# Kernel optimization log

Measured on AMD Instinct MI355X. Metric: run time of the kernel, lower is better.

Reference implementation:

```python
import jax, jax.numpy as jnp
import numpy as np

DIM = 1024
HEADS = 16
HEAD_DIM = DIM // HEADS
THETA = 10000.0


def _freqs_cis(d, n, theta=THETA):
    # complex rotary frequencies, shape (n, d//2)
    pos = jnp.arange(n, dtype=jnp.float32)
    inv = 1.0 / theta ** (jnp.arange(0, d, 2, dtype=jnp.float32) / d)
    ang = jnp.outer(pos, inv)
    return jax.lax.complex(jnp.cos(ang), jnp.sin(ang))


def _to_complex(x):
    # (..., d) -> (..., d//2) complex via adjacent pairs
    xr = x.astype(jnp.float32).reshape(*x.shape[:-1], -1, 2)
    return jax.lax.complex(xr[..., 0], xr[..., 1])


def _to_real(xc):
    # (..., d//2) complex -> (..., d) interleaved real/imag
    return jnp.stack([jnp.real(xc), jnp.imag(xc)], axis=-1).reshape(*xc.shape[:-1], -1)


def setup_inputs() -> dict:
    key = jax.random.key(0)
    k1, k2, k3 = jax.random.split(key, 3)
    b, seq = 2, 2048
    x = jax.random.normal(k1, (b, DIM, seq), dtype=jnp.float32)
    w_qkv = jax.random.normal(k2, (3 * DIM, DIM), dtype=jnp.float32) * (DIM ** -0.5)
    w_out = jax.random.normal(k3, (DIM, DIM), dtype=jnp.float32) * (DIM ** -0.5)
    return {"x": x, "w_qkv": w_qkv, "w_out": w_out}


def reference(x, w_qkv, w_out):
    b, dim, n = x.shape
    h, hd = HEADS, HEAD_DIM
    scale = hd ** -0.5
    xt = jnp.swapaxes(x, -1, -2)                      # (b, t, dim)
    qkv = jnp.einsum('btd,ed->bte', xt, w_qkv)        # (b, t, 3*dim)
    q, k, v = jnp.split(qkv, 3, axis=-1)
    q = q.reshape(b, n, h, hd)
    k = k.reshape(b, n, h, hd)
    v = v.reshape(b, n, h, hd)
    # rotary embedding on q, k
    fc = _freqs_cis(hd, n)[None, :, None, :]          # (1, t, 1, hd//2)
    q = _to_real(_to_complex(q) * fc).astype(x.dtype)
    k = _to_real(_to_complex(k) * fc).astype(x.dtype)
    # naive full attention
    logits = jnp.einsum('bqhd,bkhd->bhqk', q, k) * scale
    probs = jax.nn.softmax(logits, axis=-1)
    out = jnp.einsum('bhqk,bkhd->bqhd', probs, v)     # (b, t, h, hd)
    out = out.reshape(b, n, dim)
    out = jnp.einsum('btd,ed->bte', out, w_out)       # (b, t, dim)
    return jnp.swapaxes(out, -1, -2)                  # (b, dim, t)
```

## Files before the change

kernel.cpp:

```cpp
#include <hip/hip_runtime.h>
#include <hip/hip_bf16.h>
#include <math.h>

#define B 2
#define N 2048
#define D 1024
#define H 16
#define HD 64

typedef __attribute__((ext_vector_type(8))) short short8;
typedef __attribute__((ext_vector_type(4))) float f32x4;
typedef __attribute__((ext_vector_type(16))) float f32x16;
typedef __attribute__((ext_vector_type(4))) unsigned short ush4;
typedef __attribute__((ext_vector_type(4))) unsigned int uint4v;

__device__ __forceinline__ float bf2f(unsigned short u) {
  unsigned int x = ((unsigned int)u) << 16;
  float f;
  __builtin_memcpy(&f, &x, 4);
  return f;
}
__device__ __forceinline__ unsigned short f2bf(float f) {
  unsigned int x;
  __builtin_memcpy(&x, &f, 4);
  x = x + 0x7fffu + ((x >> 16) & 1u);
  return (unsigned short)(x >> 16);
}
__device__ __forceinline__ unsigned int pk2(float lo, float hi) {
  union { __hip_bfloat162 h; unsigned int u; } cv;
  cv.h = __float22bfloat162_rn(make_float2(lo, hi));
  return cv.u;
}
__device__ __forceinline__ short8 mk_frag(unsigned int w0, unsigned int w1,
                                          unsigned int w2, unsigned int w3) {
  union { uint4v u; short8 s; } cv;
  cv.u = (uint4v){w0, w1, w2, w3};
  return cv.s;
}

__device__ __forceinline__ void gload16(const unsigned short* g, unsigned short* l) {
  __builtin_amdgcn_global_load_lds(
      (const __attribute__((address_space(1))) unsigned int*)(const void*)g,
      (__attribute__((address_space(3))) unsigned int*)(void*)l, 16, 0, 0);
}

__global__ void conv_bf16(const float* __restrict__ src, unsigned short* __restrict__ dst, int n4) {
  int i = blockIdx.x * 256 + threadIdx.x;
  if (i >= n4) return;
  float4 v = ((const float4*)src)[i];
  ush4 o;
  o[0] = f2bf(v.x); o[1] = f2bf(v.y); o[2] = f2bf(v.z); o[3] = f2bf(v.w);
  *(ush4*)&dst[i * 4] = o;
}

__global__ __launch_bounds__(256) void transpose_x(const float* __restrict__ x,
                                                   unsigned short* __restrict__ xt) {
  __shared__ float tile[32][33];
  const int tx = threadIdx.x, ty = threadIdx.y;
  const int t0 = blockIdx.x * 32, d0 = blockIdx.y * 32, bb = blockIdx.z;
#pragma unroll
  for (int i = 0; i < 4; ++i) {
    int r = ty * 4 + i;
    tile[r][tx] = x[(size_t)bb * D * N + (size_t)(d0 + r) * N + t0 + tx];
  }
  __syncthreads();
#pragma unroll
  for (int i = 0; i < 4; ++i) {
    int r = ty * 4 + i;
    xt[((size_t)(bb * N) + t0 + r) * D + d0 + tx] = f2bf(tile[tx][r]);
  }
}

__global__ void rope_table(float2* __restrict__ tab) {
  int idx = blockIdx.x * 256 + threadIdx.x;
  int t = idx >> 5, p = idx & 31;
  float inv = powf(10000.f, -(float)p / 32.f);
  float ang = (float)t * inv;
  float s, c;
  sincosf(ang, &s, &c);
  tab[idx] = make_float2(c, s);
}

template <int MODE>
__global__ __launch_bounds__(256) void gemm_bt(const unsigned short* __restrict__ A,
                                               const unsigned short* __restrict__ Bt,
                                               float* __restrict__ outf,
                                               unsigned short* __restrict__ qkbuf,
                                               unsigned short* __restrict__ vtbuf) {
  __shared__ unsigned short Asm[128 * 64];
  __shared__ unsigned short Bsm[128 * 64];
  const int tid = threadIdx.x;
  const int lane = tid & 63, wid = tid >> 6;
  const int ln = lane & 15, lh = lane >> 4;
  const int wr = wid >> 1, wc = wid & 1;
  const int m0 = blockIdx.x * 128, n0 = blockIdx.y * 128;

  f32x4 acc[4][4];
#pragma unroll
  for (int i = 0; i < 4; ++i)
#pragma unroll
    for (int j = 0; j < 4; ++j) acc[i][j] = (f32x4){0.f, 0.f, 0.f, 0.f};

  for (int k0 = 0; k0 < 1024; k0 += 64) {
#pragma unroll
    for (int jj = 0; jj < 4; ++jj) {
      int slot = tid + jj * 256;
      int row = slot >> 3, u = slot & 7;
      int usw = (u ^ (row & 7)) * 8;
      gload16(&A[(size_t)(m0 + row) * 1024 + k0 + usw], &Asm[slot * 8]);
    }
#pragma unroll
    for (int jj = 0; jj < 4; ++jj) {
      int slot = tid + jj * 256;
      int row = slot >> 3, u = slot & 7;
      int usw = (u ^ (row & 7)) * 8;
      gload16(&Bt[(size_t)(n0 + row) * 1024 + k0 + usw], &Bsm[slot * 8]);
    }
    __syncthreads();
#pragma unroll
    for (int s = 0; s < 2; ++s) {
      short8 af[4], bfr[4];
#pragma unroll
      for (int i = 0; i < 4; ++i) {
        int row = wr * 64 + i * 16 + ln;
        int u = ((s * 4 + lh) ^ (row & 7)) * 8;
        af[i] = *(const short8*)&Asm[row * 64 + u];
      }
#pragma unroll
      for (int j = 0; j < 4; ++j) {
        int row = wc * 64 + j * 16 + ln;
        int u = ((s * 4 + lh) ^ (row & 7)) * 8;
        bfr[j] = *(const short8*)&Bsm[row * 64 + u];
      }
#pragma unroll
      for (int i = 0; i < 4; ++i)
#pragma unroll
        for (int j = 0; j < 4; ++j)
          acc[i][j] = __builtin_amdgcn_mfma_f32_16x16x32_bf16(af[i], bfr[j], acc[i][j], 0, 0, 0);
    }
    __syncthreads();
  }

#pragma unroll
  for (int i = 0; i < 4; ++i) {
    int mrow = m0 + wr * 64 + i * 16 + lh * 4;
    int bb = mrow >> 11, t = mrow & 2047;
#pragma unroll
    for (int j = 0; j < 4; ++j) {
      int e = n0 + wc * 64 + j * 16 + ln;
      if (MODE == 1) {
        float* op = outf + (size_t)bb * D * N + (size_t)e * N + t;
        *(f32x4*)op = acc[i][j];
      } else {
        if (e < 2048) {
#pragma unroll
          for (int jj = 0; jj < 4; ++jj)
            qkbuf[((size_t)(bb * N + t + jj)) * 2048 + e] = f2bf(acc[i][j][jj]);
        } else {
          ush4 v;
#pragma unroll
          for (int jj = 0; jj < 4; ++jj) v[jj] = f2bf(acc[i][j][jj]);
          *(ush4*)&vtbuf[((size_t)bb * 1024 + (e - 2048)) * N + t] = v;
        }
      }
    }
  }
}

__global__ void rope_kernel(unsigned short* __restrict__ qk, const float2* __restrict__ tab) {
  int idx = blockIdx.x * 256 + threadIdx.x;
  int e = (idx & 255) * 8;
  int t = (idx >> 8) & 2047;
  int bb = idx >> 19;
  int p0 = (e & 63) >> 1;
  const float qscl = 0.125f * 1.4426950408889634f;
  float sc = (e < 1024) ? qscl : 1.0f;
  unsigned short* p = qk + ((size_t)(bb * N + t)) * 2048 + e;
  short8 v = *(short8*)p;
#pragma unroll
  for (int q = 0; q < 4; ++q) {
    float2 cs = tab[t * 32 + p0 + q];
    float xe = bf2f((unsigned short)v[2 * q]);
    float xo = bf2f((unsigned short)v[2 * q + 1]);
    v[2 * q] = (short)f2bf((xe * cs.x - xo * cs.y) * sc);
    v[2 * q + 1] = (short)f2bf((xe * cs.y + xo * cs.x) * sc);
  }
  *(short8*)p = v;
}

__global__ __launch_bounds__(256, 2) void attn_kernel(const unsigned short* __restrict__ qk,
                                                      const unsigned short* __restrict__ vt,
                                                      unsigned short* __restrict__ ob) {
  __shared__ unsigned short Ksm[2][64 * 64];
  __shared__ unsigned short Vsm[2][64 * 64];
  const int tid = threadIdx.x;
  const int lane = tid & 63, wid = tid >> 6;
  const int l31 = lane & 31, hi = lane >> 5;
  const int L = blockIdx.x;
  const int hh = L & 31, qb = L >> 5;
  const int bb = hh >> 4, h = hh & 15;
  const unsigned short* Qg = qk + (size_t)bb * N * 2048 + h * 64;
  const unsigned short* Kg = Qg + 1024;
  const unsigned short* Vg = vt + ((size_t)bb * 1024 + h * 64) * N;

  const int q = qb * 128 + wid * 32 + l31;
  short8 qf[4];
#pragma unroll
  for (int c = 0; c < 4; ++c)
    qf[c] = *(const short8*)&Qg[(size_t)q * 2048 + c * 16 + hi * 8];

  f32x16 oL, oH;
#pragma unroll
  for (int r = 0; r < 16; ++r) { oL[r] = 0.f; oH[r] = 0.f; }
  float lrun = 0.f;

  auto STAGE = [&](int buf, int kb) {
#pragma unroll
    for (int jj = 0; jj < 2; ++jj) {
      int slot = tid + jj * 256;
      int row = slot >> 3, u = slot & 7;
      int usw = (u ^ (row & 7)) * 8;
      gload16(&Kg[(size_t)(kb + row) * 2048 + usw], &Ksm[buf][slot * 8]);
    }
#pragma unroll
    for (int jj = 0; jj < 2; ++jj) {
      int slot = tid + jj * 256;
      int row = slot >> 3, u = slot & 7;
      int usw = (u ^ (row & 7)) * 8;
      gload16(&Vg[(size_t)row * N + kb + usw], &Vsm[buf][slot * 8]);
    }
  };

  STAGE(0, 0);
  __syncthreads();
  int cur = 0;
  for (int t = 0; t < N / 64; ++t) {
    if (t < N / 64 - 1) STAGE(cur ^ 1, (t + 1) * 64);
    f32x16 s0, s1;
#pragma unroll
    for (int r = 0; r < 16; ++r) { s0[r] = 0.f; s1[r] = 0.f; }
#pragma unroll
    for (int c = 0; c < 4; ++c) {
      short8 ka = *(const short8*)&Ksm[cur][l31 * 64 + (((c * 2 + hi) ^ (l31 & 7)) * 8)];
      s0 = __builtin_amdgcn_mfma_f32_32x32x16_bf16(ka, qf[c], s0, 0, 0, 0);
      int r1 = 32 + l31;
      short8 kb2 = *(const short8*)&Ksm[cur][r1 * 64 + (((c * 2 + hi) ^ (r1 & 7)) * 8)];
      s1 = __builtin_amdgcn_mfma_f32_32x32x16_bf16(kb2, qf[c], s1, 0, 0, 0);
    }
    float lsum = 0.f;
#pragma unroll
    for (int r = 0; r < 16; ++r) {
      s0[r] = __builtin_amdgcn_exp2f(s0[r]);
      s1[r] = __builtin_amdgcn_exp2f(s1[r]);
      lsum += s0[r] + s1[r];
    }
    lrun += lsum;
    unsigned int W[16];
#pragma unroll
    for (int i = 0; i < 8; ++i) {
      W[i] = pk2(s0[2 * i], s0[2 * i + 1]);
      W[8 + i] = pk2(s1[2 * i], s1[2 * i + 1]);
    }
    short8 pf[4];
#pragma unroll
    for (int c = 0; c < 4; ++c) {
      unsigned int a0 = W[4 * c + 0], b0 = W[4 * c + 2];
      unsigned int a1 = W[4 * c + 1], b1 = W[4 * c + 3];
      asm volatile("v_permlane32_swap_b32 %0, %1" : "+v"(a0), "+v"(b0));
      asm volatile("v_permlane32_swap_b32 %0, %1" : "+v"(a1), "+v"(b1));
      pf[c] = mk_frag(a0, a1, b0, b1);
    }
#pragma unroll
    for (int c = 0; c < 4; ++c) {
      short8 va = *(const short8*)&Vsm[cur][l31 * 64 + (((c * 2 + hi) ^ (l31 & 7)) * 8)];
      oL = __builtin_amdgcn_mfma_f32_32x32x16_bf16(va, pf[c], oL, 0, 0, 0);
      int rH = 32 + l31;
      short8 vb = *(const short8*)&Vsm[cur][rH * 64 + (((c * 2 + hi) ^ (rH & 7)) * 8)];
      oH = __builtin_amdgcn_mfma_f32_32x32x16_bf16(vb, pf[c], oH, 0, 0, 0);
    }
    __syncthreads();
    cur ^= 1;
  }
  lrun += __shfl_xor(lrun, 32, 64);
  float inv = 1.f / lrun;
  unsigned short* obp = ob + ((size_t)(bb * N + q)) * 1024 + h * 64;
#pragma unroll
  for (int r4 = 0; r4 < 4; ++r4) {
    ush4 vL, vH;
#pragma unroll
    for (int i = 0; i < 4; ++i) {
      vL[i] = f2bf(oL[r4 * 4 + i] * inv);
      vH[i] = f2bf(oH[r4 * 4 + i] * inv);
    }
    *(ush4*)&obp[r4 * 8 + hi * 4] = vL;
    *(ush4*)&obp[32 + r4 * 8 + hi * 4] = vH;
  }
}

extern "C" void kernel_launch(void* const* d_in, const int* in_sizes, int n_in,
                              void* d_out, int out_size, void* d_ws, size_t ws_size,
                              hipStream_t stream) {
  const float* x = (const float*)d_in[0];
  const float* w_qkv = (const float*)d_in[1];
  const float* w_out = (const float*)d_in[2];
  float* out = (float*)d_out;
  char* ws = (char*)d_ws;

  unsigned short* wqkv_bf = (unsigned short*)ws;
  unsigned short* wout_bf = (unsigned short*)(ws + 6291456);
  unsigned short* xt      = (unsigned short*)(ws + 8388608);
  unsigned short* qkbuf   = (unsigned short*)(ws + 16777216);
  unsigned short* vtbuf   = (unsigned short*)(ws + 33554432);
  float2* tab             = (float2*)(ws + 41943040);

  conv_bf16<<<3072, 256, 0, stream>>>(w_qkv, wqkv_bf, 3072 * 1024 / 4);
  conv_bf16<<<1024, 256, 0, stream>>>(w_out, wout_bf, 1024 * 1024 / 4);
  transpose_x<<<dim3(N / 32, D / 32, B), dim3(32, 8), 0, stream>>>(x, xt);
  rope_table<<<256, 256, 0, stream>>>(tab);

  gemm_bt<0><<<dim3(32, 24), 256, 0, stream>>>(xt, wqkv_bf, nullptr, qkbuf, vtbuf);
  rope_kernel<<<4096, 256, 0, stream>>>(qkbuf, tab);
  attn_kernel<<<512, 256, 0, stream>>>(qkbuf, vtbuf, xt );
  gemm_bt<1><<<dim3(32, 8), 256, 0, stream>>>(xt, wout_bf, out, nullptr, nullptr);
}
```

Measured before the change: 132.8 us.

## Triple-buffer attention K/V loads with explicit waitcnt and fuse prep kernels

The attention loop moves from double to triple-buffered K/V staging. Each tile is prefetched two iterations ahead, using s_waitcnt vmcnt plus raw s_barrier instead of __syncthreads, and setprio raises priority around the MFMA blocks. The weight conversion and rope table kernels are merged into one launch. This is meant to hide global load latency and cut launch overhead, at the cost of 50% more LDS per block and fragile hand-counted wait counts.

```diff
diff --git a/kernel.cpp b/kernel.cpp
--- a/kernel.cpp
+++ b/kernel.cpp
@@ -44,13 +44,27 @@
       (__attribute__((address_space(3))) unsigned int*)(void*)l, 16, 0, 0);
 }
 
-__global__ void conv_bf16(const float* __restrict__ src, unsigned short* __restrict__ dst, int n4) {
-  int i = blockIdx.x * 256 + threadIdx.x;
-  if (i >= n4) return;
-  float4 v = ((const float4*)src)[i];
-  ush4 o;
-  o[0] = f2bf(v.x); o[1] = f2bf(v.y); o[2] = f2bf(v.z); o[3] = f2bf(v.w);
-  *(ush4*)&dst[i * 4] = o;
+__global__ void prep_k(const float* __restrict__ wqkv, unsigned short* __restrict__ wqkv_bf,
+                       const float* __restrict__ wout, unsigned short* __restrict__ wout_bf,
+                       float2* __restrict__ tab) {
+  int blk = blockIdx.x;
+  if (blk < 4096) {
+    const float* src = (blk < 3072) ? wqkv : wout;
+    unsigned short* dst = (blk < 3072) ? wqkv_bf : wout_bf;
+    int i = (blk < 3072 ? blk : blk - 3072) * 256 + threadIdx.x;
+    float4 v = ((const float4*)src)[i];
+    ush4 o;
+    o[0] = f2bf(v.x); o[1] = f2bf(v.y); o[2] = f2bf(v.z); o[3] = f2bf(v.w);
+    *(ush4*)&dst[i * 4] = o;
+  } else {
+    int idx = (blk - 4096) * 256 + threadIdx.x;
+    int t = idx >> 5, p = idx & 31;
+    float inv = powf(10000.f, -(float)p / 32.f);
+    float ang = (float)t * inv;
+    float s, c;
+    sincosf(ang, &s, &c);
+    tab[idx] = make_float2(c, s);
+  }
 }
 
 __global__ __launch_bounds__(256) void transpose_x(const float* __restrict__ x,
@@ -69,16 +83,6 @@
     int r = ty * 4 + i;
     xt[((size_t)(bb * N) + t0 + r) * D + d0 + tx] = f2bf(tile[tx][r]);
   }
-}
-
-__global__ void rope_table(float2* __restrict__ tab) {
-  int idx = blockIdx.x * 256 + threadIdx.x;
-  int t = idx >> 5, p = idx & 31;
-  float inv = powf(10000.f, -(float)p / 32.f);
-  float ang = (float)t * inv;
-  float s, c;
-  sincosf(ang, &s, &c);
-  tab[idx] = make_float2(c, s);
 }
 
 template <int MODE>
@@ -191,8 +195,8 @@
 __global__ __launch_bounds__(256, 2) void attn_kernel(const unsigned short* __restrict__ qk,
                                                       const unsigned short* __restrict__ vt,
                                                       unsigned short* __restrict__ ob) {
-  __shared__ unsigned short Ksm[2][64 * 64];
-  __shared__ unsigned short Vsm[2][64 * 64];
+  __shared__ unsigned short Ksm[3][64 * 64];
+  __shared__ unsigned short Vsm[3][64 * 64];
   const int tid = threadIdx.x;
   const int lane = tid & 63, wid = tid >> 6;
   const int l31 = lane & 31, hi = lane >> 5;
@@ -214,39 +218,37 @@
   for (int r = 0; r < 16; ++r) { oL[r] = 0.f; oH[r] = 0.f; }
   float lrun = 0.f;
 
-  auto STAGE = [&](int buf, int kb) {
+  auto STAGE = [&](unsigned short* Kb, unsigned short* Vb, int kb) {
 #pragma unroll
     for (int jj = 0; jj < 2; ++jj) {
       int slot = tid + jj * 256;
       int row = slot >> 3, u = slot & 7;
       int usw = (u ^ (row & 7)) * 8;
-      gload16(&Kg[(size_t)(kb + row) * 2048 + usw], &Ksm[buf][slot * 8]);
+      gload16(&Kg[(size_t)(kb + row) * 2048 + usw], &Kb[slot * 8]);
     }
 #pragma unroll
     for (int jj = 0; jj < 2; ++jj) {
       int slot = tid + jj * 256;
       int row = slot >> 3, u = slot & 7;
       int usw = (u ^ (row & 7)) * 8;
-      gload16(&Vg[(size_t)row * N + kb + usw], &Vsm[buf][slot * 8]);
+      gload16(&Vg[(size_t)row * N + kb + usw], &Vb[slot * 8]);
     }
   };
 
-  STAGE(0, 0);
-  __syncthreads();
-  int cur = 0;
-  for (int t = 0; t < N / 64; ++t) {
-    if (t < N / 64 - 1) STAGE(cur ^ 1, (t + 1) * 64);
+  auto COMPUTE = [&](const unsigned short* Kb, const unsigned short* Vb) {
     f32x16 s0, s1;
 #pragma unroll
     for (int r = 0; r < 16; ++r) { s0[r] = 0.f; s1[r] = 0.f; }
+    __builtin_amdgcn_s_setprio(1);
 #pragma unroll
     for (int c = 0; c < 4; ++c) {
-      short8 ka = *(const short8*)&Ksm[cur][l31 * 64 + (((c * 2 + hi) ^ (l31 & 7)) * 8)];
+      short8 ka = *(const short8*)&Kb[l31 * 64 + (((c * 2 + hi) ^ (l31 & 7)) * 8)];
       s0 = __builtin_amdgcn_mfma_f32_32x32x16_bf16(ka, qf[c], s0, 0, 0, 0);
       int r1 = 32 + l31;
-      short8 kb2 = *(const short8*)&Ksm[cur][r1 * 64 + (((c * 2 + hi) ^ (r1 & 7)) * 8)];
+      short8 kb2 = *(const short8*)&Kb[r1 * 64 + (((c * 2 + hi) ^ (r1 & 7)) * 8)];
       s1 = __builtin_amdgcn_mfma_f32_32x32x16_bf16(kb2, qf[c], s1, 0, 0, 0);
     }
+    __builtin_amdgcn_s_setprio(0);
     float lsum = 0.f;
 #pragma unroll
     for (int r = 0; r < 16; ++r) {
@@ -270,17 +272,44 @@
       asm volatile("v_permlane32_swap_b32 %0, %1" : "+v"(a1), "+v"(b1));
       pf[c] = mk_frag(a0, a1, b0, b1);
     }
+    __builtin_amdgcn_s_setprio(1);
 #pragma unroll
     for (int c = 0; c < 4; ++c) {
-      short8 va = *(const short8*)&Vsm[cur][l31 * 64 + (((c * 2 + hi) ^ (l31 & 7)) * 8)];
+      short8 va = *(const short8*)&Vb[l31 * 64 + (((c * 2 + hi) ^ (l31 & 7)) * 8)];
       oL = __builtin_amdgcn_mfma_f32_32x32x16_bf16(va, pf[c], oL, 0, 0, 0);
       int rH = 32 + l31;
-      short8 vb = *(const short8*)&Vsm[cur][rH * 64 + (((c * 2 + hi) ^ (rH & 7)) * 8)];
+      short8 vb = *(const short8*)&Vb[rH * 64 + (((c * 2 + hi) ^ (rH & 7)) * 8)];
       oH = __builtin_amdgcn_mfma_f32_32x32x16_bf16(vb, pf[c], oH, 0, 0, 0);
     }
-    __syncthreads();
-    cur ^= 1;
-  }
+    __builtin_amdgcn_s_setprio(0);
+  };
+
+  auto ITER = [&](int t, int bc, int bn) {
+    __builtin_amdgcn_s_barrier();
+    STAGE(Ksm[bn], Vsm[bn], (t + 2) * 64);
+    asm volatile("s_waitcnt vmcnt(8)" ::: "memory");
+    __builtin_amdgcn_sched_barrier(0);
+    __builtin_amdgcn_s_barrier();
+    COMPUTE(Ksm[bc], Vsm[bc]);
+  };
+
+  STAGE(Ksm[0], Vsm[0], 0);
+  STAGE(Ksm[1], Vsm[1], 64);
+  for (int tt = 0; tt < 30; tt += 3) {
+    ITER(tt + 0, 0, 2);
+    ITER(tt + 1, 1, 0);
+    ITER(tt + 2, 2, 1);
+  }
+  __builtin_amdgcn_s_barrier();
+  asm volatile("s_waitcnt vmcnt(4)" ::: "memory");
+  __builtin_amdgcn_sched_barrier(0);
+  __builtin_amdgcn_s_barrier();
+  COMPUTE(Ksm[0], Vsm[0]);
+  asm volatile("s_waitcnt vmcnt(0)" ::: "memory");
+  __builtin_amdgcn_sched_barrier(0);
+  __builtin_amdgcn_s_barrier();
+  COMPUTE(Ksm[1], Vsm[1]);
+
   lrun += __shfl_xor(lrun, 32, 64);
   float inv = 1.f / lrun;
   unsigned short* obp = ob + ((size_t)(bb * N + q)) * 1024 + h * 64;
@@ -313,10 +342,8 @@
   unsigned short* vtbuf   = (unsigned short*)(ws + 33554432);
   float2* tab             = (float2*)(ws + 41943040);
 
-  conv_bf16<<<3072, 256, 0, stream>>>(w_qkv, wqkv_bf, 3072 * 1024 / 4);
-  conv_bf16<<<1024, 256, 0, stream>>>(w_out, wout_bf, 1024 * 1024 / 4);
+  prep_k<<<4352, 256, 0, stream>>>(w_qkv, wqkv_bf, w_out, wout_bf, tab);
   transpose_x<<<dim3(N / 32, D / 32, B), dim3(32, 8), 0, stream>>>(x, xt);
-  rope_table<<<256, 256, 0, stream>>>(tab);
 
   gemm_bt<0><<<dim3(32, 24), 256, 0, stream>>>(xt, wqkv_bf, nullptr, qkbuf, vtbuf);
   rope_kernel<<<4096, 256, 0, stream>>>(qkbuf, tab);
```

After: 127.6 us. 1.04x faster.

## Fuse RoPE into QKV GEMM epilogue, merge prep kernels, add MFMA setprio

Applied to the files above, without the earlier changes.

The separate RoPE pass is folded into the QKV GEMM epilogue. Q/K tiles are staged in swizzled shared memory, rotated with the table, scaled, and written as coalesced 16-byte rows. This removes a full read/write pass over the Q/K buffer and the scattered 2-byte epilogue stores. The weight conversions and the rope table build are merged into one launch. The attention MFMA sections are wrapped in s_setprio to favour matrix issue across waves.

```diff
diff --git a/kernel.cpp b/kernel.cpp
--- a/kernel.cpp
+++ b/kernel.cpp
@@ -9,6 +9,7 @@
 #define HD 64
 
 typedef __attribute__((ext_vector_type(8))) short short8;
+typedef __attribute__((ext_vector_type(8))) unsigned short ush8;
 typedef __attribute__((ext_vector_type(4))) float f32x4;
 typedef __attribute__((ext_vector_type(16))) float f32x16;
 typedef __attribute__((ext_vector_type(4))) unsigned short ush4;
@@ -44,13 +45,27 @@
       (__attribute__((address_space(3))) unsigned int*)(void*)l, 16, 0, 0);
 }
 
-__global__ void conv_bf16(const float* __restrict__ src, unsigned short* __restrict__ dst, int n4) {
-  int i = blockIdx.x * 256 + threadIdx.x;
-  if (i >= n4) return;
-  float4 v = ((const float4*)src)[i];
-  ush4 o;
-  o[0] = f2bf(v.x); o[1] = f2bf(v.y); o[2] = f2bf(v.z); o[3] = f2bf(v.w);
-  *(ush4*)&dst[i * 4] = o;
+__global__ void prep_k(const float* __restrict__ wqkv, unsigned short* __restrict__ wqkv_bf,
+                       const float* __restrict__ wout, unsigned short* __restrict__ wout_bf,
+                       float2* __restrict__ tab) {
+  int blk = blockIdx.x;
+  if (blk < 4096) {
+    const float* src = (blk < 3072) ? wqkv : wout;
+    unsigned short* dst = (blk < 3072) ? wqkv_bf : wout_bf;
+    int i = (blk < 3072 ? blk : blk - 3072) * 256 + threadIdx.x;
+    float4 v = ((const float4*)src)[i];
+    ush4 o;
+    o[0] = f2bf(v.x); o[1] = f2bf(v.y); o[2] = f2bf(v.z); o[3] = f2bf(v.w);
+    *(ush4*)&dst[i * 4] = o;
+  } else {
+    int idx = (blk - 4096) * 256 + threadIdx.x;
+    int t = idx >> 5, p = idx & 31;
+    float inv = powf(10000.f, -(float)p / 32.f);
+    float ang = (float)t * inv;
+    float s, c;
+    sincosf(ang, &s, &c);
+    tab[idx] = make_float2(c, s);
+  }
 }
 
 __global__ __launch_bounds__(256) void transpose_x(const float* __restrict__ x,
@@ -71,24 +86,16 @@
   }
 }
 
-__global__ void rope_table(float2* __restrict__ tab) {
-  int idx = blockIdx.x * 256 + threadIdx.x;
-  int t = idx >> 5, p = idx & 31;
-  float inv = powf(10000.f, -(float)p / 32.f);
-  float ang = (float)t * inv;
-  float s, c;
-  sincosf(ang, &s, &c);
-  tab[idx] = make_float2(c, s);
-}
-
 template <int MODE>
 __global__ __launch_bounds__(256) void gemm_bt(const unsigned short* __restrict__ A,
                                                const unsigned short* __restrict__ Bt,
                                                float* __restrict__ outf,
                                                unsigned short* __restrict__ qkbuf,
-                                               unsigned short* __restrict__ vtbuf) {
-  __shared__ unsigned short Asm[128 * 64];
-  __shared__ unsigned short Bsm[128 * 64];
+                                               unsigned short* __restrict__ vtbuf,
+                                               const float2* __restrict__ tab) {
+  __shared__ __align__(16) unsigned short smem_all[128 * 128];
+  unsigned short* Asm = smem_all;
+  unsigned short* Bsm = smem_all + 128 * 64;
   const int tid = threadIdx.x;
   const int lane = tid & 63, wid = tid >> 6;
   const int ln = lane & 15, lh = lane >> 4;
@@ -141,21 +148,52 @@
     __syncthreads();
   }
 
-#pragma unroll
-  for (int i = 0; i < 4; ++i) {
-    int mrow = m0 + wr * 64 + i * 16 + lh * 4;
-    int bb = mrow >> 11, t = mrow & 2047;
-#pragma unroll
-    for (int j = 0; j < 4; ++j) {
-      int e = n0 + wc * 64 + j * 16 + ln;
-      if (MODE == 1) {
-        float* op = outf + (size_t)bb * D * N + (size_t)e * N + t;
-        *(f32x4*)op = acc[i][j];
-      } else {
-        if (e < 2048) {
-#pragma unroll
-          for (int jj = 0; jj < 4; ++jj)
-            qkbuf[((size_t)(bb * N + t + jj)) * 2048 + e] = f2bf(acc[i][j][jj]);
+  if (MODE == 0 && n0 < 2048) {
+    unsigned short* Csm = smem_all;
+#pragma unroll
+    for (int i = 0; i < 4; ++i) {
+      int rb = wr * 64 + i * 16 + lh * 4;
+#pragma unroll
+      for (int j = 0; j < 4; ++j) {
+        int e = wc * 64 + j * 16 + ln;
+        int c = e >> 3, o = e & 7;
+#pragma unroll
+        for (int jj = 0; jj < 4; ++jj) {
+          int rr = rb + jj;
+          Csm[rr * 128 + ((c ^ (rr & 15)) * 8) + o] = f2bf(acc[i][j][jj]);
+        }
+      }
+    }
+    __syncthreads();
+    const int bb = m0 >> 11, tbase = m0 & 2047;
+    const float sc = (n0 < 1024) ? 0.125f * 1.4426950408889634f : 1.0f;
+    const int c16 = tid & 15, rgrp = tid >> 4;
+    const int p0 = (c16 & 7) * 4;
+#pragma unroll
+    for (int pass = 0; pass < 8; ++pass) {
+      int r = rgrp + pass * 16;
+      int t = tbase + r;
+      ush8 v = *(const ush8*)&Csm[r * 128 + ((c16 ^ rgrp) * 8)];
+#pragma unroll
+      for (int k = 0; k < 4; ++k) {
+        float2 cs = tab[t * 32 + p0 + k];
+        float xe = bf2f(v[2 * k]), xo = bf2f(v[2 * k + 1]);
+        v[2 * k]     = f2bf((xe * cs.x - xo * cs.y) * sc);
+        v[2 * k + 1] = f2bf((xe * cs.y + xo * cs.x) * sc);
+      }
+      *(ush8*)&qkbuf[((size_t)(bb * N + t)) * 2048 + n0 + c16 * 8] = v;
+    }
+  } else {
+#pragma unroll
+    for (int i = 0; i < 4; ++i) {
+      int mrow = m0 + wr * 64 + i * 16 + lh * 4;
+      int bb = mrow >> 11, t = mrow & 2047;
+#pragma unroll
+      for (int j = 0; j < 4; ++j) {
+        int e = n0 + wc * 64 + j * 16 + ln;
+        if (MODE == 1) {
+          float* op = outf + (size_t)bb * D * N + (size_t)e * N + t;
+          *(f32x4*)op = acc[i][j];
         } else {
           ush4 v;
 #pragma unroll
@@ -165,27 +203,6 @@
       }
     }
   }
-}
-
-__global__ void rope_kernel(unsigned short* __restrict__ qk, const float2* __restrict__ tab) {
-  int idx = blockIdx.x * 256 + threadIdx.x;
-  int e = (idx & 255) * 8;
-  int t = (idx >> 8) & 2047;
-  int bb = idx >> 19;
-  int p0 = (e & 63) >> 1;
-  const float qscl = 0.125f * 1.4426950408889634f;
-  float sc = (e < 1024) ? qscl : 1.0f;
-  unsigned short* p = qk + ((size_t)(bb * N + t)) * 2048 + e;
-  short8 v = *(short8*)p;
-#pragma unroll
-  for (int q = 0; q < 4; ++q) {
-    float2 cs = tab[t * 32 + p0 + q];
-    float xe = bf2f((unsigned short)v[2 * q]);
-    float xo = bf2f((unsigned short)v[2 * q + 1]);
-    v[2 * q] = (short)f2bf((xe * cs.x - xo * cs.y) * sc);
-    v[2 * q + 1] = (short)f2bf((xe * cs.y + xo * cs.x) * sc);
-  }
-  *(short8*)p = v;
 }
 
 __global__ __launch_bounds__(256, 2) void attn_kernel(const unsigned short* __restrict__ qk,
@@ -239,6 +256,7 @@
     f32x16 s0, s1;
 #pragma unroll
     for (int r = 0; r < 16; ++r) { s0[r] = 0.f; s1[r] = 0.f; }
+    __builtin_amdgcn_s_setprio(1);
 #pragma unroll
     for (int c = 0; c < 4; ++c) {
       short8 ka = *(const short8*)&Ksm[cur][l31 * 64 + (((c * 2 + hi) ^ (l31 & 7)) * 8)];
@@ -247,6 +265,7 @@
       short8 kb2 = *(const short8*)&Ksm[cur][r1 * 64 + (((c * 2 + hi) ^ (r1 & 7)) * 8)];
       s1 = __builtin_amdgcn_mfma_f32_32x32x16_bf16(kb2, qf[c], s1, 0, 0, 0);
     }
+    __builtin_amdgcn_s_setprio(0);
     float lsum = 0.f;
 #pragma unroll
     for (int r = 0; r < 16; ++r) {
@@ -270,6 +289,7 @@
       asm volatile("v_permlane32_swap_b32 %0, %1" : "+v"(a1), "+v"(b1));
       pf[c] = mk_frag(a0, a1, b0, b1);
     }
+    __builtin_amdgcn_s_setprio(1);
 #pragma unroll
     for (int c = 0; c < 4; ++c) {
       short8 va = *(const short8*)&Vsm[cur][l31 * 64 + (((c * 2 + hi) ^ (l31 & 7)) * 8)];
@@ -278,6 +298,7 @@
       short8 vb = *(const short8*)&Vsm[cur][rH * 64 + (((c * 2 + hi) ^ (rH & 7)) * 8)];
       oH = __builtin_amdgcn_mfma_f32_32x32x16_bf16(vb, pf[c], oH, 0, 0, 0);
     }
+    __builtin_amdgcn_s_setprio(0);
     __syncthreads();
     cur ^= 1;
   }
@@ -313,13 +334,10 @@
   unsigned short* vtbuf   = (unsigned short*)(ws + 33554432);
   float2* tab             = (float2*)(ws + 41943040);
 
-  conv_bf16<<<3072, 256, 0, stream>>>(w_qkv, wqkv_bf, 3072 * 1024 / 4);
-  conv_bf16<<<1024, 256, 0, stream>>>(w_out, wout_bf, 1024 * 1024 / 4);
+  prep_k<<<4352, 256, 0, stream>>>(w_qkv, wqkv_bf, w_out, wout_bf, tab);
   transpose_x<<<dim3(N / 32, D / 32, B), dim3(32, 8), 0, stream>>>(x, xt);
-  rope_table<<<256, 256, 0, stream>>>(tab);
-
-  gemm_bt<0><<<dim3(32, 24), 256, 0, stream>>>(xt, wqkv_bf, nullptr, qkbuf, vtbuf);
-  rope_kernel<<<4096, 256, 0, stream>>>(qkbuf, tab);
+
+  gemm_bt<0><<<dim3(32, 24), 256, 0, stream>>>(xt, wqkv_bf, nullptr, qkbuf, vtbuf, tab);
   attn_kernel<<<512, 256, 0, stream>>>(qkbuf, vtbuf, xt );
-  gemm_bt<1><<<dim3(32, 8), 256, 0, stream>>>(xt, wout_bf, out, nullptr, nullptr);
-}
+  gemm_bt<1><<<dim3(32, 8), 256, 0, stream>>>(xt, wout_bf, out, nullptr, nullptr, nullptr);
+}
```

Measured after the change: 128.7 us. 3.1% less time.
